# Performance work log

Hardware: AMD Instinct MI355X
Metric: run time of the kernel (lower is better)

The kernel has to match this reference:

```python
import jax, jax.numpy as jnp
import numpy as np

STRIDE, PAD, DIL, K = 1, 1, 1, 3  # from init_kwargs; kernel hardcoded 3x3 in module


def setup_inputs() -> dict:
    key = jax.random.key(0)
    k1, k2, k3, k4, k5 = jax.random.split(key, 5)
    B, C, H, W, O = 8, 128, 64, 64, 128
    inp = jax.random.normal(k1, (B, C, H, W), jnp.float32)
    # offsets in pixels; small magnitudes are typical of learned DCN offsets
    offset = jax.random.normal(k2, (B, 2 * K * K, H, W), jnp.float32)
    mask = jax.random.uniform(k3, (B, K * K, H, W), dtype=jnp.float32)  # modulation in [0,1)
    weight = jax.random.normal(k4, (O, C, K, K), jnp.float32) * 0.05
    bias = jax.random.normal(k5, (O,), jnp.float32) * 0.05
    return {"input": inp, "offset": offset, "mask": mask, "weight": weight, "bias": bias}


def reference(input, offset, mask, weight, bias):
    B, C, H, W = input.shape
    O = weight.shape[0]
    Ho = (H + 2 * PAD - DIL * (K - 1) - 1) // STRIDE + 1
    Wo = (W + 2 * PAD - DIL * (K - 1) - 1) // STRIDE + 1

    # torchvision layout: offset[:, 2k] = dy, offset[:, 2k+1] = dx for kernel tap k
    off = offset.reshape(B, K * K, 2, Ho, Wo)
    off_y, off_x = off[:, :, 0], off[:, :, 1]  # [B, 9, Ho, Wo]

    kh, kw = jnp.meshgrid(jnp.arange(K), jnp.arange(K), indexing="ij")
    kh, kw = kh.reshape(-1), kw.reshape(-1)  # [9]

    # absolute (fractional) sampling positions per output pixel and kernel tap
    py = (jnp.arange(Ho) * STRIDE - PAD)[None, None, :, None] + (kh * DIL)[None, :, None, None] + off_y
    px = (jnp.arange(Wo) * STRIDE - PAD)[None, None, None, :] + (kw * DIL)[None, :, None, None] + off_x

    y0 = jnp.floor(py)
    x0 = jnp.floor(px)
    wy1 = py - y0  # fractional parts
    wx1 = px - x0

    inp_bhwc = jnp.transpose(input, (0, 2, 3, 1))  # [B, H, W, C] for clean gather
    b_idx = jnp.arange(B)[:, None, None, None]

    def corner(yc, xc, w):
        # zero-padded bilinear: out-of-bounds corners contribute 0
        valid = (yc >= 0) & (yc < H) & (xc >= 0) & (xc < W)
        ycl = jnp.clip(yc, 0, H - 1).astype(jnp.int32)
        xcl = jnp.clip(xc, 0, W - 1).astype(jnp.int32)
        v = inp_bhwc[b_idx, ycl, xcl]  # [B, 9, Ho, Wo, C]
        return v * (w * valid)[..., None]

    sampled = (corner(y0, x0, (1 - wy1) * (1 - wx1))
               + corner(y0, x0 + 1, (1 - wy1) * wx1)
               + corner(y0 + 1, x0, wy1 * (1 - wx1))
               + corner(y0 + 1, x0 + 1, wy1 * wx1))  # [B, 9, Ho, Wo, C]

    sampled = sampled * mask[..., None]  # DCNv2 modulation

    out = jnp.einsum("bkhwc,ock->bohw", sampled, weight.reshape(O, C, K * K))
    return out + bias[None, :, None, None]
```

## Files before the change

### kernel.cpp

```cpp
#include <hip/hip_runtime.h>

#define BB 8
#define CC 128
#define HH 64
#define WW 64
#define OO 128
#define KT 9
#define HWs (HH * WW)

typedef __attribute__((ext_vector_type(8))) _Float16 half8;
typedef __attribute__((ext_vector_type(8))) short short8;
typedef __attribute__((ext_vector_type(4))) float f32x4;

__device__ inline unsigned short f2bf(float f) {
    union { float f; unsigned int u; } x; x.f = f;
    unsigned int u = x.u;
    unsigned int r = u + 0x7fff + ((u >> 16) & 1);
    return (unsigned short)(r >> 16);
}

__device__ __forceinline__ void gload_lds16(const void* g, void* l) {
    __builtin_amdgcn_global_load_lds(
        (__attribute__((address_space(1))) void*)g,
        (__attribute__((address_space(3))) void*)l, 16, 0, 0);
}

__global__ __launch_bounds__(256) void prep_input(
    const float* __restrict__ in, _Float16* __restrict__ out) {
    __shared__ float t[CC][33];
    int b = blockIdx.y;
    int s0 = blockIdx.x * 32;
    int s = threadIdx.x & 31;
    int c0 = threadIdx.x >> 5;
    const float* ip = in + (size_t)b * CC * HWs;
#pragma unroll
    for (int c = 0; c < CC; c += 8)
        t[c + c0][s] = ip[(size_t)(c + c0) * HWs + s0 + s];
    __syncthreads();
    int ws = threadIdx.x >> 3;
    int cg = (threadIdx.x & 7) * 16;
    _Float16 v[16];
#pragma unroll
    for (int i = 0; i < 16; ++i) v[i] = (_Float16)t[cg + i][ws];
    _Float16* op = out + ((size_t)(b * HWs) + s0 + ws) * CC + cg;
    *(half8*)op = *(half8*)&v[0];
    *(half8*)(op + 8) = *(half8*)&v[8];
}

__global__ __launch_bounds__(256) void prep_weight(
    const float* __restrict__ w, unsigned short* __restrict__ wbf) {
    int i = blockIdx.x * 256 + threadIdx.x;
    if (i >= KT * OO * CC) return;
    int k = i / (OO * CC);
    int r = i % (OO * CC);
    int o = r >> 7, c = r & 127;
    unsigned byte = (unsigned)(o * 256 + ((2 * c) ^ ((o & 15) << 4)));
    *(unsigned short*)((char*)wbf + (size_t)k * 32768 + byte) =
        f2bf(w[o * (CC * KT) + c * KT + k]);
}

struct GatherR {
    half8 g[8];
    float w00, w01, w10, w11;
};

__device__ __forceinline__ void sample_issue(
    const _Float16* __restrict__ base, int ho, int wo, int cs, int k,
    float oy, float ox, float mm, GatherR& G) {
    int kh = k / 3, kw = k % 3;
    float py = (float)(ho - 1 + kh) + oy;
    float px = (float)(wo - 1 + kw) + ox;
    float fy = floorf(py), fx = floorf(px);
    float wy1 = py - fy, wx1 = px - fx;
    float wy0 = 1.f - wy1, wx0 = 1.f - wx1;
    int y0 = (int)fy, x0 = (int)fx;
    int y1 = y0 + 1, x1 = x0 + 1;
    bool vy0 = (y0 >= 0) & (y0 < HH);
    bool vy1 = (y1 >= 0) & (y1 < HH);
    bool vx0 = (x0 >= 0) & (x0 < WW);
    bool vx1 = (x1 >= 0) & (x1 < WW);
    G.w00 = (vy0 & vx0) ? wy0 * wx0 * mm : 0.f;
    G.w01 = (vy0 & vx1) ? wy0 * wx1 * mm : 0.f;
    G.w10 = (vy1 & vx0) ? wy1 * wx0 * mm : 0.f;
    G.w11 = (vy1 & vx1) ? wy1 * wx1 * mm : 0.f;
    int y0c = min(max(y0, 0), HH - 1), y1c = min(max(y1, 0), HH - 1);
    int x0c = min(max(x0, 0), WW - 1), x1c = min(max(x1, 0), WW - 1);
    const _Float16* p00 = base + (size_t)(y0c * WW + x0c) * CC + cs;
    const _Float16* p01 = base + (size_t)(y0c * WW + x1c) * CC + cs;
    const _Float16* p10 = base + (size_t)(y1c * WW + x0c) * CC + cs;
    const _Float16* p11 = base + (size_t)(y1c * WW + x1c) * CC + cs;
    G.g[0] = *(const half8*)p00;  G.g[1] = *(const half8*)(p00 + 32);
    G.g[2] = *(const half8*)p01;  G.g[3] = *(const half8*)(p01 + 32);
    G.g[4] = *(const half8*)p10;  G.g[5] = *(const half8*)(p10 + 32);
    G.g[6] = *(const half8*)p11;  G.g[7] = *(const half8*)(p11 + 32);
}

__global__ __launch_bounds__(256, 2) void deform_main(
    const _Float16* __restrict__ inh, const unsigned short* __restrict__ wbf,
    const float* __restrict__ offset, const float* __restrict__ mask,
    const float* __restrict__ bias, float* __restrict__ out) {
    __shared__ unsigned short Bl[OO * CC];

    int hw = blockIdx.x;
    int lb = (hw & 7) * 128 + (hw >> 3);
    int b = lb >> 7;
    int rem = lb & 127;
    int ho = rem >> 1;
    int px0 = (rem & 1) * 32;

    int tid = threadIdx.x;
    int wv = tid >> 6, l = tid & 63;
    int lr = l & 15, lg = l >> 4;
    int p = wv >> 1;
    int khalf = wv & 1;
    int wo = px0 + p * 16 + lr;
    int cs = khalf * 64 + lg * 8;

    const _Float16* base = inh + (size_t)b * HWs * CC;
    const float* offp = offset + (size_t)b * 18 * HWs + ho * WW + wo;
    const float* mskp = mask + (size_t)b * 9 * HWs + ho * WW + wo;

    const char* wsrc = (const char*)wbf + (size_t)wv * 8192 + (size_t)l * 16;
    char* ldst = (char*)Bl + wv * 8192;

    f32x4 acc[8] = {};
    GatherR G;

    {
        float oy = offp[0], ox = offp[HWs], mm = mskp[0];
        sample_issue(base, ho, wo, cs, 0, oy, ox, mm, G);
    }
    float oyN = offp[2 * HWs], oxN = offp[3 * HWs], mmN = mskp[HWs];

    for (int k = 0; k < KT; ++k) {
        short8 af[2];
#pragma unroll
        for (int cc = 0; cc < 2; ++cc)
#pragma unroll
            for (int j = 0; j < 8; ++j) {
                float s = G.w00 * (float)G.g[0 * 2 + cc][j] +
                          G.w01 * (float)G.g[1 * 2 + cc][j] +
                          G.w10 * (float)G.g[2 * 2 + cc][j] +
                          G.w11 * (float)G.g[3 * 2 + cc][j];
                af[cc][j] = (short)f2bf(s);
            }

        __syncthreads();

        {
            const char* s = wsrc + (size_t)k * 32768;
#pragma unroll
            for (int j = 0; j < 8; ++j)
                gload_lds16(s + j * 1024, ldst + j * 1024);
        }
        __syncthreads();

        if (k < KT - 1) {
            sample_issue(base, ho, wo, cs, k + 1, oyN, oxN, mmN, G);
            if (k < KT - 2) {
                oyN = offp[(2 * k + 4) * HWs];
                oxN = offp[(2 * k + 5) * HWs];
                mmN = mskp[(k + 2) * HWs];
            }
        }

#pragma unroll
        for (int cc = 0; cc < 2; ++cc) {
            unsigned colb = (unsigned)((khalf * 2 + cc) * 64 + lg * 16);
#pragma unroll
            for (int n = 0; n < 8; ++n) {
                int o = n * 16 + lr;
                unsigned baddr = (unsigned)(o * 256 + (colb ^ (lr << 4)));
                short8 bf = *(const short8*)((const char*)Bl + baddr);
                acc[n] = __builtin_amdgcn_mfma_f32_16x16x32_bf16(
                    af[cc], bf, acc[n], 0, 0, 0);
            }
        }
    }

    __syncthreads();
    float* L = (float*)Bl;
    if (khalf) {
#pragma unroll
        for (int n = 0; n < 8; ++n)
#pragma unroll
            for (int j = 0; j < 4; ++j)
                L[(size_t)(p * 16 + lg * 4 + j) * 128 + n * 16 + lr] = acc[n][j];
    }
    __syncthreads();
    if (!khalf) {
#pragma unroll
        for (int n = 0; n < 8; ++n) {
            int o = n * 16 + lr;
            float bs = bias[o];
            float4 v;
            v.x = acc[n][0] + bs + L[(size_t)(p * 16 + lg * 4 + 0) * 128 + o];
            v.y = acc[n][1] + bs + L[(size_t)(p * 16 + lg * 4 + 1) * 128 + o];
            v.z = acc[n][2] + bs + L[(size_t)(p * 16 + lg * 4 + 2) * 128 + o];
            v.w = acc[n][3] + bs + L[(size_t)(p * 16 + lg * 4 + 3) * 128 + o];
            int wo0 = px0 + p * 16 + lg * 4;
            *(float4*)(out + (size_t)(b * OO + o) * HWs + ho * WW + wo0) = v;
        }
    }
}

extern "C" void kernel_launch(void* const* d_in, const int* in_sizes, int n_in,
                              void* d_out, int out_size, void* d_ws, size_t ws_size,
                              hipStream_t stream) {
    const float* inp    = (const float*)d_in[0];
    const float* offset = (const float*)d_in[1];
    const float* mask   = (const float*)d_in[2];
    const float* weight = (const float*)d_in[3];
    const float* bias   = (const float*)d_in[4];
    float* out = (float*)d_out;

    _Float16* inh = (_Float16*)d_ws;
    unsigned short* wbf =
        (unsigned short*)((char*)d_ws + (size_t)BB * HWs * CC * sizeof(_Float16));

    prep_input<<<dim3(128, 8), 256, 0, stream>>>(inp, inh);
    prep_weight<<<dim3((KT * OO * CC + 255) / 256), 256, 0, stream>>>(weight, wbf);
    deform_main<<<dim3(1024), 256, 0, stream>>>(inh, wbf, offset, mask, bias, out);
}
```

Baseline: 63.71 us.

## Split fused deform conv into separate sampling kernel and im2col GEMM kernel

Replaces the fused gather-plus-MFMA kernel with two kernels. The first bilinearly samples every tap and writes a swizzled bf16 im2col matrix to workspace. The second runs a 64-row tiled GEMM against the weights, loading A and B through direct global-to-LDS copies. This drops the cross-wave K-split reduction and decouples gather latency from MFMA work, at the cost of a large intermediate buffer written and read through global memory (about 75 MB for all batches), plus extra launches when the workspace forces batch chunking.

```diff
diff --git a/kernel.cpp b/kernel.cpp
--- a/kernel.cpp
+++ b/kernel.cpp
@@ -10,6 +10,7 @@
 
 typedef __attribute__((ext_vector_type(8))) _Float16 half8;
 typedef __attribute__((ext_vector_type(8))) short short8;
+typedef __attribute__((ext_vector_type(8))) unsigned short ushort8;
 typedef __attribute__((ext_vector_type(4))) float f32x4;
 
 __device__ inline unsigned short f2bf(float f) {
@@ -59,19 +60,34 @@
         f2bf(w[o * (CC * KT) + c * KT + k]);
 }
 
-struct GatherR {
-    half8 g[8];
-    float w00, w01, w10, w11;
-};
-
-__device__ __forceinline__ void sample_issue(
-    const _Float16* __restrict__ base, int ho, int wo, int cs, int k,
-    float oy, float ox, float mm, GatherR& G) {
-    int kh = k / 3, kw = k % 3;
+__global__ __launch_bounds__(256, 2) void deform_sample(
+    const _Float16* __restrict__ inh, const float* __restrict__ offset,
+    const float* __restrict__ mask, unsigned short* __restrict__ As,
+    int b0, int lnb) {
+    int nb = 1 << lnb;
+    int hw = blockIdx.x;
+    int xcd = hw & 7;
+    int j = hw >> 3;
+    int bl = xcd & (nb - 1);
+    int task = (xcd >> lnb) * (144 << lnb) + j;
+    int tap = task >> 7;
+    int blk = task & 127;
+    int tid = threadIdx.x;
+    int px = blk * 32 + (tid >> 3);
+    int cg = (tid & 7) * 16;
+    int ho = px >> 6, wo = px & 63;
+    int b = b0 + bl;
+
+    const _Float16* base = inh + (size_t)b * HWs * CC;
+    float oy = offset[(size_t)(b * 18 + 2 * tap) * HWs + ho * WW + wo];
+    float ox = offset[(size_t)(b * 18 + 2 * tap + 1) * HWs + ho * WW + wo];
+    float mm = mask[(size_t)(b * 9 + tap) * HWs + ho * WW + wo];
+
+    int kh = tap / 3, kw = tap % 3;
     float py = (float)(ho - 1 + kh) + oy;
-    float px = (float)(wo - 1 + kw) + ox;
-    float fy = floorf(py), fx = floorf(px);
-    float wy1 = py - fy, wx1 = px - fx;
+    float pxf = (float)(wo - 1 + kw) + ox;
+    float fy = floorf(py), fx = floorf(pxf);
+    float wy1 = py - fy, wx1 = pxf - fx;
     float wy0 = 1.f - wy1, wx0 = 1.f - wx1;
     int y0 = (int)fy, x0 = (int)fx;
     int y1 = y0 + 1, x1 = x0 + 1;
@@ -79,128 +95,106 @@
     bool vy1 = (y1 >= 0) & (y1 < HH);
     bool vx0 = (x0 >= 0) & (x0 < WW);
     bool vx1 = (x1 >= 0) & (x1 < WW);
-    G.w00 = (vy0 & vx0) ? wy0 * wx0 * mm : 0.f;
-    G.w01 = (vy0 & vx1) ? wy0 * wx1 * mm : 0.f;
-    G.w10 = (vy1 & vx0) ? wy1 * wx0 * mm : 0.f;
-    G.w11 = (vy1 & vx1) ? wy1 * wx1 * mm : 0.f;
+    float w00 = (vy0 & vx0) ? wy0 * wx0 * mm : 0.f;
+    float w01 = (vy0 & vx1) ? wy0 * wx1 * mm : 0.f;
+    float w10 = (vy1 & vx0) ? wy1 * wx0 * mm : 0.f;
+    float w11 = (vy1 & vx1) ? wy1 * wx1 * mm : 0.f;
     int y0c = min(max(y0, 0), HH - 1), y1c = min(max(y1, 0), HH - 1);
     int x0c = min(max(x0, 0), WW - 1), x1c = min(max(x1, 0), WW - 1);
-    const _Float16* p00 = base + (size_t)(y0c * WW + x0c) * CC + cs;
-    const _Float16* p01 = base + (size_t)(y0c * WW + x1c) * CC + cs;
-    const _Float16* p10 = base + (size_t)(y1c * WW + x0c) * CC + cs;
-    const _Float16* p11 = base + (size_t)(y1c * WW + x1c) * CC + cs;
-    G.g[0] = *(const half8*)p00;  G.g[1] = *(const half8*)(p00 + 32);
-    G.g[2] = *(const half8*)p01;  G.g[3] = *(const half8*)(p01 + 32);
-    G.g[4] = *(const half8*)p10;  G.g[5] = *(const half8*)(p10 + 32);
-    G.g[6] = *(const half8*)p11;  G.g[7] = *(const half8*)(p11 + 32);
-}
-
-__global__ __launch_bounds__(256, 2) void deform_main(
-    const _Float16* __restrict__ inh, const unsigned short* __restrict__ wbf,
-    const float* __restrict__ offset, const float* __restrict__ mask,
-    const float* __restrict__ bias, float* __restrict__ out) {
+    const _Float16* p00 = base + (size_t)(y0c * WW + x0c) * CC + cg;
+    const _Float16* p01 = base + (size_t)(y0c * WW + x1c) * CC + cg;
+    const _Float16* p10 = base + (size_t)(y1c * WW + x0c) * CC + cg;
+    const _Float16* p11 = base + (size_t)(y1c * WW + x1c) * CC + cg;
+    half8 g00a = *(const half8*)p00, g00b = *(const half8*)(p00 + 8);
+    half8 g01a = *(const half8*)p01, g01b = *(const half8*)(p01 + 8);
+    half8 g10a = *(const half8*)p10, g10b = *(const half8*)(p10 + 8);
+    half8 g11a = *(const half8*)p11, g11b = *(const half8*)(p11 + 8);
+
+    ushort8 o0, o1;
+#pragma unroll
+    for (int q = 0; q < 8; ++q) {
+        float s = w00 * (float)g00a[q] + w01 * (float)g01a[q] +
+                  w10 * (float)g10a[q] + w11 * (float)g11a[q];
+        o0[q] = f2bf(s);
+    }
+#pragma unroll
+    for (int q = 0; q < 8; ++q) {
+        float s = w00 * (float)g00b[q] + w01 * (float)g01b[q] +
+                  w10 * (float)g10b[q] + w11 * (float)g11b[q];
+        o1[q] = f2bf(s);
+    }
+    char* rowp = (char*)As + ((size_t)bl * 4096 + px) * 2304 + tap * 256;
+    unsigned sw = (unsigned)((px & 15) << 4);
+    *(ushort8*)(rowp + ((2 * cg) ^ sw)) = o0;
+    *(ushort8*)(rowp + ((2 * cg + 16) ^ sw)) = o1;
+}
+
+__global__ __launch_bounds__(256, 2) void deform_gemm(
+    const unsigned short* __restrict__ As, const unsigned short* __restrict__ wbf,
+    const float* __restrict__ bias, float* __restrict__ out, int b0) {
+    __shared__ unsigned short Al[64 * 128];
     __shared__ unsigned short Bl[OO * CC];
 
-    int hw = blockIdx.x;
-    int lb = (hw & 7) * 128 + (hw >> 3);
-    int b = lb >> 7;
-    int rem = lb & 127;
-    int ho = rem >> 1;
-    int px0 = (rem & 1) * 32;
-
+    int bpx = blockIdx.x * 64;
     int tid = threadIdx.x;
     int wv = tid >> 6, l = tid & 63;
     int lr = l & 15, lg = l >> 4;
-    int p = wv >> 1;
-    int khalf = wv & 1;
-    int wo = px0 + p * 16 + lr;
-    int cs = khalf * 64 + lg * 8;
-
-    const _Float16* base = inh + (size_t)b * HWs * CC;
-    const float* offp = offset + (size_t)b * 18 * HWs + ho * WW + wo;
-    const float* mskp = mask + (size_t)b * 9 * HWs + ho * WW + wo;
-
-    const char* wsrc = (const char*)wbf + (size_t)wv * 8192 + (size_t)l * 16;
-    char* ldst = (char*)Bl + wv * 8192;
+
+    const char* bwsrc = (const char*)wbf + (size_t)wv * 8192 + (size_t)l * 16;
+    char* bldst = (char*)Bl + wv * 8192;
 
     f32x4 acc[8] = {};
-    GatherR G;
-
-    {
-        float oy = offp[0], ox = offp[HWs], mm = mskp[0];
-        sample_issue(base, ho, wo, cs, 0, oy, ox, mm, G);
-    }
-    float oyN = offp[2 * HWs], oxN = offp[3 * HWs], mmN = mskp[HWs];
 
     for (int k = 0; k < KT; ++k) {
-        short8 af[2];
-#pragma unroll
-        for (int cc = 0; cc < 2; ++cc)
-#pragma unroll
-            for (int j = 0; j < 8; ++j) {
-                float s = G.w00 * (float)G.g[0 * 2 + cc][j] +
-                          G.w01 * (float)G.g[1 * 2 + cc][j] +
-                          G.w10 * (float)G.g[2 * 2 + cc][j] +
-                          G.w11 * (float)G.g[3 * 2 + cc][j];
-                af[cc][j] = (short)f2bf(s);
+        __syncthreads();
+        {
+            const char* s = bwsrc + (size_t)k * 32768;
+#pragma unroll
+            for (int j2 = 0; j2 < 8; ++j2)
+                gload_lds16(s + j2 * 1024, bldst + j2 * 1024);
+        }
+        {
+#pragma unroll
+            for (int j2 = 0; j2 < 4; ++j2) {
+                int row = wv * 16 + j2 * 4 + lg;
+                const char* s = (const char*)As +
+                    (size_t)(bpx + row) * 2304 + (size_t)k * 256 + lr * 16;
+                gload_lds16(s, (char*)Al + (wv * 16 + j2 * 4) * 256);
             }
-
-        __syncthreads();
-
-        {
-            const char* s = wsrc + (size_t)k * 32768;
-#pragma unroll
-            for (int j = 0; j < 8; ++j)
-                gload_lds16(s + j * 1024, ldst + j * 1024);
         }
         __syncthreads();
 
-        if (k < KT - 1) {
-            sample_issue(base, ho, wo, cs, k + 1, oyN, oxN, mmN, G);
-            if (k < KT - 2) {
-                oyN = offp[(2 * k + 4) * HWs];
-                oxN = offp[(2 * k + 5) * HWs];
-                mmN = mskp[(k + 2) * HWs];
+#pragma unroll
+        for (int c32 = 0; c32 < 4; ++c32) {
+            int arow = wv * 16 + lr;
+            unsigned ab = (unsigned)(arow * 256 + ((c32 * 64 + lg * 16) ^ (lr << 4)));
+            short8 af = *(const short8*)((const char*)Al + ab);
+#pragma unroll
+            for (int n = 0; n < 8; ++n) {
+                int o = n * 16 + lr;
+                unsigned bb = (unsigned)(o * 256 + ((c32 * 64 + lg * 16) ^ (lr << 4)));
+                short8 bf = *(const short8*)((const char*)Bl + bb);
+                acc[n] = __builtin_amdgcn_mfma_f32_16x16x32_bf16(
+                    af, bf, acc[n], 0, 0, 0);
             }
         }
-
-#pragma unroll
-        for (int cc = 0; cc < 2; ++cc) {
-            unsigned colb = (unsigned)((khalf * 2 + cc) * 64 + lg * 16);
-#pragma unroll
-            for (int n = 0; n < 8; ++n) {
-                int o = n * 16 + lr;
-                unsigned baddr = (unsigned)(o * 256 + (colb ^ (lr << 4)));
-                short8 bf = *(const short8*)((const char*)Bl + baddr);
-                acc[n] = __builtin_amdgcn_mfma_f32_16x16x32_bf16(
-                    af[cc], bf, acc[n], 0, 0, 0);
-            }
-        }
-    }
-
-    __syncthreads();
-    float* L = (float*)Bl;
-    if (khalf) {
-#pragma unroll
-        for (int n = 0; n < 8; ++n)
-#pragma unroll
-            for (int j = 0; j < 4; ++j)
-                L[(size_t)(p * 16 + lg * 4 + j) * 128 + n * 16 + lr] = acc[n][j];
-    }
-    __syncthreads();
-    if (!khalf) {
-#pragma unroll
-        for (int n = 0; n < 8; ++n) {
-            int o = n * 16 + lr;
-            float bs = bias[o];
-            float4 v;
-            v.x = acc[n][0] + bs + L[(size_t)(p * 16 + lg * 4 + 0) * 128 + o];
-            v.y = acc[n][1] + bs + L[(size_t)(p * 16 + lg * 4 + 1) * 128 + o];
-            v.z = acc[n][2] + bs + L[(size_t)(p * 16 + lg * 4 + 2) * 128 + o];
-            v.w = acc[n][3] + bs + L[(size_t)(p * 16 + lg * 4 + 3) * 128 + o];
-            int wo0 = px0 + p * 16 + lg * 4;
-            *(float4*)(out + (size_t)(b * OO + o) * HWs + ho * WW + wo0) = v;
-        }
+    }
+
+    int sp0 = bpx + wv * 16 + lg * 4;
+    int b = b0 + (sp0 >> 12);
+    int sp = sp0 & 4095;
+    int ho = sp >> 6;
+    int wo0 = sp & 63;
+#pragma unroll
+    for (int n = 0; n < 8; ++n) {
+        int o = n * 16 + lr;
+        float bs = bias[o];
+        float4 v;
+        v.x = acc[n][0] + bs;
+        v.y = acc[n][1] + bs;
+        v.z = acc[n][2] + bs;
+        v.w = acc[n][3] + bs;
+        *(float4*)(out + (size_t)(b * OO + o) * HWs + ho * WW + wo0) = v;
     }
 }
 
@@ -214,11 +208,22 @@
     const float* bias   = (const float*)d_in[4];
     float* out = (float*)d_out;
 
+    const size_t inh_b = (size_t)BB * HWs * CC * sizeof(_Float16);
+    const size_t wbf_b = (size_t)KT * OO * CC * sizeof(unsigned short);
     _Float16* inh = (_Float16*)d_ws;
-    unsigned short* wbf =
-        (unsigned short*)((char*)d_ws + (size_t)BB * HWs * CC * sizeof(_Float16));
+    unsigned short* wbf = (unsigned short*)((char*)d_ws + inh_b);
+    unsigned short* As = (unsigned short*)((char*)d_ws + inh_b + wbf_b);
+
+    size_t avail = (ws_size > inh_b + wbf_b) ? ws_size - inh_b - wbf_b : 0;
+    int lnb = 3;
+    while (lnb > 0 && ((size_t)(1 << lnb)) * 4096u * 2304u > avail) --lnb;
+    int nb = 1 << lnb;
 
     prep_input<<<dim3(128, 8), 256, 0, stream>>>(inp, inh);
     prep_weight<<<dim3((KT * OO * CC + 255) / 256), 256, 0, stream>>>(weight, wbf);
-    deform_main<<<dim3(1024), 256, 0, stream>>>(inh, wbf, offset, mask, bias, out);
-}
+    for (int b0 = 0; b0 < BB; b0 += nb) {
+        deform_sample<<<dim3(nb * 1152), 256, 0, stream>>>(
+            inh, offset, mask, As, b0, lnb);
+        deform_gemm<<<dim3(nb * 64), 256, 0, stream>>>(As, wbf, bias, out, b0);
+    }
+}
```

Result: faster. 53.85 us (-15.5%).
